# Performance work log

Hardware: AMD Instinct MI355X
Metric: run time of the kernel (lower is better)

The kernel has to match this reference:

```python
import jax, jax.numpy as jnp
import numpy as np

B, S, D, H = 2, 2048, 1024, 16
HD = D // H

def setup_inputs() -> dict:
    key = jax.random.key(0)
    ks = jax.random.split(key, 5)
    sc = 1.0 / np.sqrt(D)
    return {
        "x": jax.random.normal(ks[0], (B, S, D), dtype=jnp.float32),
        "Wq": jax.random.normal(ks[1], (D, D), dtype=jnp.float32) * sc,
        "bq": jnp.zeros((D,), jnp.float32),
        "Wk": jax.random.normal(ks[2], (D, D), dtype=jnp.float32) * sc,
        "bk": jnp.zeros((D,), jnp.float32),
        "Wv": jax.random.normal(ks[3], (D, D), dtype=jnp.float32) * sc,
        "bv": jnp.zeros((D,), jnp.float32),
        "Wo": jax.random.normal(ks[4], (D, D), dtype=jnp.float32) * sc,
        "bo": jnp.zeros((D,), jnp.float32),
    }

def reference(x, Wq, bq, Wk, bk, Wv, bv, Wo, bo):
    b, s, d = x.shape
    def proj(W, bias):
        # [B,S,D] -> [B,H,S,HD]
        return (x @ W + bias).reshape(b, s, H, HD).swapaxes(1, 2)
    q = proj(Wq, bq)
    k = proj(Wk, bk)
    v = proj(Wv, bv)
    # naive full attention, matching the module (materializes [B,H,S,S])
    logits = jnp.einsum("bhqd,bhkd->bhqk", q, k) / jnp.sqrt(jnp.float32(HD))
    attn = jax.nn.softmax(logits, axis=-1)
    vals = jnp.einsum("bhqk,bhkd->bhqd", attn, v)
    vals = vals.swapaxes(1, 2).reshape(b, s, d)
    return vals @ Wo + bo
```

## Files before the change

### kernel.cpp

```cpp
#include <hip/hip_runtime.h>

typedef unsigned short u16;
typedef __bf16 bf16x8 __attribute__((ext_vector_type(8)));
typedef __bf16 bf16x4 __attribute__((ext_vector_type(4)));
typedef float f32x4 __attribute__((ext_vector_type(4)));

__device__ __forceinline__ u16 f2bf(float f) {
    union { float f; unsigned int i; } v;
    v.f = f;
    unsigned int u = v.i;
    return (u16)((u + 0x7fffu + ((u >> 16) & 1u)) >> 16);
}

__device__ __forceinline__ void dma16(const void* g, void* l) {
    __builtin_amdgcn_global_load_lds(
        (__attribute__((address_space(1))) void*)g,
        (__attribute__((address_space(3))) void*)l, 16, 0, 0);
}


__global__ __launch_bounds__(256) void cvt_w4(
    const float* __restrict__ W0, const float* __restrict__ W1,
    const float* __restrict__ W2, const float* __restrict__ W3,
    u16* __restrict__ out) {
    __shared__ u16 t[32][33];
    int z = blockIdx.z;
    const float* in = (z == 0) ? W0 : (z == 1) ? W1 : (z == 2) ? W2 : W3;
    u16* o = out + (size_t)z * 1048576;
    int bx = blockIdx.x * 32, by = blockIdx.y * 32;
    int tx = threadIdx.x & 31, ty = threadIdx.x >> 5;
#pragma unroll
    for (int i = 0; i < 32; i += 8)
        t[ty + i][tx] = f2bf(in[(size_t)(by + ty + i) * 1024 + bx + tx]);
    __syncthreads();
#pragma unroll
    for (int i = 0; i < 32; i += 8) {
        int n = bx + ty + i, k = by + tx;
        o[(size_t)n * 1024 + (k ^ ((n & 7) << 3))] = t[tx][ty + i];
    }
}

__global__ __launch_bounds__(256) void cvt_x(const float* __restrict__ in,
                                             u16* __restrict__ out) {
    int i = blockIdx.x * 256 + threadIdx.x;
    int s = i >> 8, k = (i & 255) * 4;
    float4 f = reinterpret_cast<const float4*>(in)[i];
    ushort4 h;
    h.x = f2bf(f.x); h.y = f2bf(f.y); h.z = f2bf(f.z); h.w = f2bf(f.w);
    *reinterpret_cast<ushort4*>(&out[(size_t)s * 1024 + (k ^ ((s & 7) << 3))]) = h;
}

__global__ __launch_bounds__(256) void gemm_qkv(
    const u16* __restrict__ xbf, const u16* __restrict__ wt,
    const float* __restrict__ bq, const float* __restrict__ bk,
    const float* __restrict__ bv,
    u16* __restrict__ qkg, u16* __restrict__ vgt) {
    __shared__ __align__(16) u16 As[128 * 64];
    __shared__ __align__(16) u16 Bs[128 * 64];

    int tid = threadIdx.x;
    int m0 = blockIdx.y * 128, n0 = blockIdx.x * 128;
    int wave = tid >> 6, lane = tid & 63;
    int wm = (wave >> 1) * 64, wn = (wave & 1) * 64;
    int l16 = lane & 15, quad = lane >> 4;
    int sl = l16 & 7;

    int seg = n0 >> 10;
    int n0r = n0 & 1023;
    const u16* WT = wt + (size_t)seg * 1048576;
    bool swp = (seg == 2);

    f32x4 acc[4][4];
#pragma unroll
    for (int mi = 0; mi < 4; mi++)
#pragma unroll
        for (int ni = 0; ni < 4; ni++) acc[mi][ni] = (f32x4){0.f, 0.f, 0.f, 0.f};

    int rsub = lane >> 3, c16 = (lane & 7) * 8;
    for (int k0 = 0; k0 < 1024; k0 += 64) {
#pragma unroll
        for (int i = 0; i < 4; i++) {
            int row = wave * 32 + i * 8 + rsub;
            dma16(&xbf[(size_t)(m0 + row) * 1024 + k0 + c16], &As[wave * 2048 + i * 512]);
            dma16(&WT[(size_t)(n0r + row) * 1024 + k0 + c16], &Bs[wave * 2048 + i * 512]);
        }
        __syncthreads();
        const u16* Am = swp ? Bs : As;
        const u16* Bn = swp ? As : Bs;
#pragma unroll
        for (int kk = 0; kk < 64; kk += 32) {
            int co = ((((kk >> 3) + quad) ^ sl) << 3);
            bf16x8 af[4], bf[4];
#pragma unroll
            for (int mi = 0; mi < 4; mi++)
                af[mi] = *reinterpret_cast<const bf16x8*>(
                    &Am[(wm + mi * 16 + l16) * 64 + co]);
#pragma unroll
            for (int ni = 0; ni < 4; ni++)
                bf[ni] = *reinterpret_cast<const bf16x8*>(
                    &Bn[(wn + ni * 16 + l16) * 64 + co]);
#pragma unroll
            for (int mi = 0; mi < 4; mi++)
#pragma unroll
                for (int ni = 0; ni < 4; ni++)
                    acc[mi][ni] = __builtin_amdgcn_mfma_f32_16x16x32_bf16(
                        af[mi], bf[ni], acc[mi][ni], 0, 0, 0);
        }
        __syncthreads();
    }

    if (!swp) {
#pragma unroll
        for (int ni = 0; ni < 4; ni++) {
            int n = n0 + wn + ni * 16 + l16;
            float bb = (n < 1024) ? bq[n] : bk[n - 1024];
#pragma unroll
            for (int mi = 0; mi < 4; mi++)
#pragma unroll
                for (int r = 0; r < 4; r++) {
                    int s = m0 + wm + mi * 16 + quad * 4 + r;
                    int key = (seg == 0) ? (s & 7) : ((s >> 2) & 7);
                    int col = n ^ (key << 3);
                    qkg[(size_t)(s >> 11) * 4194304 + (size_t)(s & 2047) * 2048 + col] =
                        f2bf(acc[mi][ni][r] + bb);
                }
        }
    } else {
#pragma unroll
        for (int mi = 0; mi < 4; mi++)
#pragma unroll
            for (int r = 0; r < 4; r++) {
                int v = n0r + wm + mi * 16 + quad * 4 + r;
                float bb = bv[v];
#pragma unroll
                for (int ni = 0; ni < 4; ni++) {
                    int s = m0 + wn + ni * 16 + l16;
                    int scol = (s & 2047) ^ ((v & 7) << 3);
                    vgt[(size_t)((s >> 11) * 1024 + v) * 2048 + scol] =
                        f2bf(acc[mi][ni][r] + bb);
                }
            }
    }
}

#define SC2 0.18033688f

__global__ __launch_bounds__(256) void attention_kern(
    u16* __restrict__ qkg, const u16* __restrict__ vgt) {
    __shared__ __align__(16) u16 Qs[64 * 64];
    __shared__ __align__(16) u16 Ks[64 * 64];
    __shared__ __align__(16) u16 Vt[64 * 64];
    __shared__ __align__(16) u16 Ps[64 * 64];

    int tid = threadIdx.x;
    int qt = blockIdx.x, h = blockIdx.y, b = blockIdx.z;
    int wave = tid >> 6, lane = tid & 63;
    int l16 = lane & 15, quad = lane >> 4;
    int rsub = lane >> 3, c16 = (lane & 7) * 8;
    int sl = l16 & 7;

    u16* qb = qkg + (size_t)b * 4194304 + (size_t)(qt * 64) * 2048 + h * 64;
    const u16* kb = qkg + (size_t)b * 4194304 + 1024 + h * 64;
    const u16* vb = vgt + (size_t)(b * 1024 + h * 64) * 2048;

#pragma unroll
    for (int i = 0; i < 2; i++) {
        int row = wave * 16 + i * 8 + rsub;
        dma16(&qb[(size_t)row * 2048 + c16], &Qs[wave * 1024 + i * 512]);
    }

    float lp[4];
    f32x4 o[4];
#pragma unroll
    for (int r = 0; r < 4; r++) lp[r] = 0.f;
#pragma unroll
    for (int ni = 0; ni < 4; ni++) o[ni] = (f32x4){0.f, 0.f, 0.f, 0.f};

    for (int kt = 0; kt < 32; kt++) {
        const u16* ktb = kb + (size_t)(kt * 64) * 2048;
        const u16* vtb = vb + kt * 64;
#pragma unroll
        for (int i = 0; i < 2; i++) {
            int gk = 32 * i + 4 * rsub + wave;
            dma16(&ktb[(size_t)gk * 2048 + c16], &Ks[wave * 1024 + i * 512]);
            int rv = wave * 16 + i * 8 + rsub;
            dma16(&vtb[(size_t)rv * 2048 + c16], &Vt[wave * 1024 + i * 512]);
        }
        __syncthreads();

        f32x4 s[4];
#pragma unroll
        for (int ni = 0; ni < 4; ni++) s[ni] = (f32x4){0.f, 0.f, 0.f, 0.f};
#pragma unroll
        for (int kk = 0; kk < 64; kk += 32) {
            int co = ((((kk >> 3) + quad) ^ sl) << 3);
            bf16x8 af = *reinterpret_cast<const bf16x8*>(
                &Qs[(wave * 16 + l16) * 64 + co]);
#pragma unroll
            for (int ni = 0; ni < 4; ni++) {
                bf16x8 bf = *reinterpret_cast<const bf16x8*>(
                    &Ks[(ni * 16 + l16) * 64 + co]);
                s[ni] = __builtin_amdgcn_mfma_f32_16x16x32_bf16(af, bf, s[ni], 0, 0, 0);
            }
        }

#pragma unroll
        for (int r = 0; r < 4; r++) {
            float p0 = __builtin_amdgcn_exp2f(s[0][r] * SC2);
            float p1 = __builtin_amdgcn_exp2f(s[1][r] * SC2);
            float p2 = __builtin_amdgcn_exp2f(s[2][r] * SC2);
            float p3 = __builtin_amdgcn_exp2f(s[3][r] * SC2);
            lp[r] += (p0 + p1) + (p2 + p3);
            f32x4 pf = {p0, p1, p2, p3};
            bf16x4 pb = __builtin_convertvector(pf, bf16x4);
            int q = wave * 16 + quad * 4 + r;
            *reinterpret_cast<bf16x4*>(
                &Ps[q * 64 + (((l16 >> 1) ^ (q & 7)) << 3) + (l16 & 1) * 4]) = pb;
        }

#pragma unroll
        for (int kk = 0; kk < 64; kk += 32) {
            int co = ((((kk >> 3) + quad) ^ sl) << 3);
            bf16x8 af = *reinterpret_cast<const bf16x8*>(
                &Ps[(wave * 16 + l16) * 64 + co]);
#pragma unroll
            for (int ni = 0; ni < 4; ni++) {
                bf16x8 bf = *reinterpret_cast<const bf16x8*>(
                    &Vt[(ni * 16 + l16) * 64 + co]);
                o[ni] = __builtin_amdgcn_mfma_f32_16x16x32_bf16(af, bf, o[ni], 0, 0, 0);
            }
        }
        __syncthreads();
    }

    float inv[4];
#pragma unroll
    for (int r = 0; r < 4; r++) {
        float v = lp[r];
#pragma unroll
        for (int off = 1; off < 16; off <<= 1) v += __shfl_xor(v, off);
        inv[r] = __builtin_amdgcn_rcpf(v);
    }
#pragma unroll
    for (int ni = 0; ni < 4; ni++)
#pragma unroll
        for (int r = 0; r < 4; r++) {
            int s = qt * 64 + wave * 16 + quad * 4 + r;
            int d = h * 64 + ni * 16 + l16;
            qkg[(size_t)b * 4194304 + (size_t)s * 2048 + (d ^ ((s & 7) << 3))] =
                f2bf(o[ni][r] * inv[r]);
        }
}

__global__ __launch_bounds__(256) void gemm_out(
    const u16* __restrict__ attb, const u16* __restrict__ wot,
    const float* __restrict__ bo, float* __restrict__ out) {
    __shared__ __align__(16) u16 As[128 * 64];
    __shared__ __align__(16) u16 Bs[64 * 64];

    int tid = threadIdx.x;
    int m0 = blockIdx.y * 128, n0 = blockIdx.x * 64;
    int wave = tid >> 6, lane = tid & 63;
    int wm = (wave >> 1) * 64, wn = (wave & 1) * 32;
    int l16 = lane & 15, quad = lane >> 4;
    int sl = l16 & 7;
    int rsub = lane >> 3, c16 = (lane & 7) * 8;

    f32x4 acc[4][2];
#pragma unroll
    for (int mi = 0; mi < 4; mi++)
#pragma unroll
        for (int ni = 0; ni < 2; ni++) acc[mi][ni] = (f32x4){0.f, 0.f, 0.f, 0.f};

    for (int k0 = 0; k0 < 1024; k0 += 64) {
#pragma unroll
        for (int i = 0; i < 4; i++) {
            int row = wave * 32 + i * 8 + rsub;
            dma16(&attb[(size_t)(m0 + row) * 2048 + k0 + c16], &As[wave * 2048 + i * 512]);
        }
#pragma unroll
        for (int i = 0; i < 2; i++) {
            int row = wave * 16 + i * 8 + rsub;
            dma16(&wot[(size_t)(n0 + row) * 1024 + k0 + c16], &Bs[wave * 1024 + i * 512]);
        }
        __syncthreads();
#pragma unroll
        for (int kk = 0; kk < 64; kk += 32) {
            int co = ((((kk >> 3) + quad) ^ sl) << 3);
            bf16x8 af[4], bf[2];
#pragma unroll
            for (int mi = 0; mi < 4; mi++)
                af[mi] = *reinterpret_cast<const bf16x8*>(
                    &As[(wm + mi * 16 + l16) * 64 + co]);
#pragma unroll
            for (int ni = 0; ni < 2; ni++)
                bf[ni] = *reinterpret_cast<const bf16x8*>(
                    &Bs[(wn + ni * 16 + l16) * 64 + co]);
#pragma unroll
            for (int mi = 0; mi < 4; mi++)
#pragma unroll
                for (int ni = 0; ni < 2; ni++)
                    acc[mi][ni] = __builtin_amdgcn_mfma_f32_16x16x32_bf16(
                        af[mi], bf[ni], acc[mi][ni], 0, 0, 0);
        }
        __syncthreads();
    }

#pragma unroll
    for (int ni = 0; ni < 2; ni++) {
        int n = n0 + wn + ni * 16 + l16;
        float bb = bo[n];
#pragma unroll
        for (int mi = 0; mi < 4; mi++)
#pragma unroll
            for (int r = 0; r < 4; r++)
                out[(size_t)(m0 + wm + mi * 16 + quad * 4 + r) * 1024 + n] =
                    acc[mi][ni][r] + bb;
    }
}

extern "C" void kernel_launch(void* const* d_in, const int* in_sizes, int n_in,
                              void* d_out, int out_size, void* d_ws, size_t ws_size,
                              hipStream_t stream) {
    const float* x  = (const float*)d_in[0];
    const float* Wq = (const float*)d_in[1];
    const float* bq = (const float*)d_in[2];
    const float* Wk = (const float*)d_in[3];
    const float* bk = (const float*)d_in[4];
    const float* Wv = (const float*)d_in[5];
    const float* bv = (const float*)d_in[6];
    const float* Wo = (const float*)d_in[7];
    const float* bo = (const float*)d_in[8];

    u16* WT  = (u16*)d_out;
    u16* xbf = (u16*)d_out + 4 * 1048576;
    u16* QKg = (u16*)d_ws;
    u16* Vgt = (u16*)d_ws + 8 * 1048576;

    cvt_w4<<<dim3(32, 32, 4), 256, 0, stream>>>(Wq, Wk, Wv, Wo, WT);
    cvt_x<<<4096, 256, 0, stream>>>(x, xbf);

    gemm_qkv<<<dim3(24, 32), 256, 0, stream>>>(xbf, WT, bq, bk, bv, QKg, Vgt);

    attention_kern<<<dim3(32, 16, 2), 256, 0, stream>>>(QKg, Vgt);

    hipMemcpyAsync(Vgt, WT + 3 * 1048576, (size_t)2 * 1048576,
                   hipMemcpyDeviceToDevice, stream);
    gemm_out<<<dim3(16, 32), 256, 0, stream>>>(QKg, Vgt, bo, (float*)d_out);
}
```

Baseline: 212.5 us.

## Double-buffer K/V tiles in attention and keep Q fragments in registers

The attention kernel now prefetches the next K and V tiles into a second LDS buffer while the current tile is being computed. It uses manual vmcnt waits and barriers in place of __syncthreads. Q is loaded once straight into registers, using the swizzled column layout, instead of being staged through LDS. This is meant to hide global-load latency behind the MFMA and softmax work, at the cost of extra LDS for the second buffers and reliance on hand-written waitcnt counts being correct.

```diff
diff --git a/kernel.cpp b/kernel.cpp
--- a/kernel.cpp
+++ b/kernel.cpp
@@ -147,9 +147,8 @@
 
 __global__ __launch_bounds__(256) void attention_kern(
     u16* __restrict__ qkg, const u16* __restrict__ vgt) {
-    __shared__ __align__(16) u16 Qs[64 * 64];
-    __shared__ __align__(16) u16 Ks[64 * 64];
-    __shared__ __align__(16) u16 Vt[64 * 64];
+    __shared__ __align__(16) u16 Ks[2][64 * 64];
+    __shared__ __align__(16) u16 Vt[2][64 * 64];
     __shared__ __align__(16) u16 Ps[64 * 64];
 
     int tid = threadIdx.x;
@@ -163,10 +162,11 @@
     const u16* kb = qkg + (size_t)b * 4194304 + 1024 + h * 64;
     const u16* vb = vgt + (size_t)(b * 1024 + h * 64) * 2048;
 
-#pragma unroll
-    for (int i = 0; i < 2; i++) {
-        int row = wave * 16 + i * 8 + rsub;
-        dma16(&qb[(size_t)row * 2048 + c16], &Qs[wave * 1024 + i * 512]);
+    bf16x8 qf[2];
+    {
+        const u16* qr = qb + (size_t)(wave * 16 + l16) * 2048;
+        qf[0] = *reinterpret_cast<const bf16x8*>(&qr[(quad ^ sl) << 3]);
+        qf[1] = *reinterpret_cast<const bf16x8*>(&qr[((4 + quad) ^ sl) << 3]);
     }
 
     float lp[4];
@@ -176,17 +176,28 @@
 #pragma unroll
     for (int ni = 0; ni < 4; ni++) o[ni] = (f32x4){0.f, 0.f, 0.f, 0.f};
 
-    for (int kt = 0; kt < 32; kt++) {
+    auto STAGE = [&](int kt, int bi) {
         const u16* ktb = kb + (size_t)(kt * 64) * 2048;
         const u16* vtb = vb + kt * 64;
 #pragma unroll
         for (int i = 0; i < 2; i++) {
             int gk = 32 * i + 4 * rsub + wave;
-            dma16(&ktb[(size_t)gk * 2048 + c16], &Ks[wave * 1024 + i * 512]);
+            dma16(&ktb[(size_t)gk * 2048 + c16], &Ks[bi][wave * 1024 + i * 512]);
             int rv = wave * 16 + i * 8 + rsub;
-            dma16(&vtb[(size_t)rv * 2048 + c16], &Vt[wave * 1024 + i * 512]);
-        }
-        __syncthreads();
+            dma16(&vtb[(size_t)rv * 2048 + c16], &Vt[bi][wave * 1024 + i * 512]);
+        }
+    };
+
+    STAGE(0, 0);
+
+    for (int kt = 0; kt < 32; kt++) {
+        int cur = kt & 1;
+        if (kt < 31) {
+            STAGE(kt + 1, cur ^ 1);
+            asm volatile("s_waitcnt vmcnt(4)\n\ts_barrier" ::: "memory");
+        } else {
+            asm volatile("s_waitcnt vmcnt(0)\n\ts_barrier" ::: "memory");
+        }
 
         f32x4 s[4];
 #pragma unroll
@@ -194,13 +205,12 @@
 #pragma unroll
         for (int kk = 0; kk < 64; kk += 32) {
             int co = ((((kk >> 3) + quad) ^ sl) << 3);
-            bf16x8 af = *reinterpret_cast<const bf16x8*>(
-                &Qs[(wave * 16 + l16) * 64 + co]);
+            bf16x8 af = qf[kk >> 5];
 #pragma unroll
             for (int ni = 0; ni < 4; ni++) {
-                bf16x8 bf = *reinterpret_cast<const bf16x8*>(
-                    &Ks[(ni * 16 + l16) * 64 + co]);
-                s[ni] = __builtin_amdgcn_mfma_f32_16x16x32_bf16(af, bf, s[ni], 0, 0, 0);
+                bf16x8 bfr = *reinterpret_cast<const bf16x8*>(
+                    &Ks[cur][(ni * 16 + l16) * 64 + co]);
+                s[ni] = __builtin_amdgcn_mfma_f32_16x16x32_bf16(af, bfr, s[ni], 0, 0, 0);
             }
         }
 
@@ -225,12 +235,12 @@
                 &Ps[(wave * 16 + l16) * 64 + co]);
 #pragma unroll
             for (int ni = 0; ni < 4; ni++) {
-                bf16x8 bf = *reinterpret_cast<const bf16x8*>(
-                    &Vt[(ni * 16 + l16) * 64 + co]);
-                o[ni] = __builtin_amdgcn_mfma_f32_16x16x32_bf16(af, bf, o[ni], 0, 0, 0);
+                bf16x8 bfr = *reinterpret_cast<const bf16x8*>(
+                    &Vt[cur][(ni * 16 + l16) * 64 + co]);
+                o[ni] = __builtin_amdgcn_mfma_f32_16x16x32_bf16(af, bfr, o[ni], 0, 0, 0);
             }
         }
-        __syncthreads();
+        asm volatile("s_waitcnt lgkmcnt(0)\n\ts_barrier" ::: "memory");
     }
 
     float inv[4];
```

After: 216.9 us. 1.02x slower.
